# Kernel optimization log

Hardware: AMD Instinct MI355X
Metric: run time of the kernel (lower is better)

Reference implementation:

```python
import math
import jax, jax.numpy as jnp
import numpy as np

B, N, C = 2, 21760, 256
L, Hh, P = 4, 8, 4
Dh = C // Hh


def setup_inputs() -> dict:
    key = jax.random.key(0)
    ks = jax.random.split(key, 8)
    shapes = np.array([[128, 128], [64, 64], [32, 32], [16, 16]], dtype=np.int64)
    areas = shapes[:, 0] * shapes[:, 1]
    start_ids = np.concatenate([[0], np.cumsum(areas)[:-1]]).astype(np.int64)
    S = int(areas.sum())  # 21760

    in_feats = jax.random.normal(ks[0], (B, N, C), jnp.float32)
    sample_priors = jax.random.uniform(ks[1], (B, N, L, 2), jnp.float32)
    sample_feats = jax.random.normal(ks[2], (B, S, C), jnp.float32)

    # sampling_offsets: zero-init weight in torch; use small random so offsets vary,
    # bias is the canonical deformable-DETR grid init.
    W_off = jax.random.normal(ks[3], (C, Hh * L * P * 2), jnp.float32) * 0.01
    thetas = jnp.arange(Hh, dtype=jnp.float32) * (2.0 * math.pi / Hh)
    grid = jnp.stack([jnp.cos(thetas), jnp.sin(thetas)], axis=1)  # [Hh,2]
    grid = grid / jnp.max(jnp.abs(grid), axis=1, keepdims=True)
    grid = jnp.tile(grid[:, None, None, :], (1, L, P, 1))  # [Hh,L,P,2]
    sizes = jnp.arange(1, P + 1, dtype=jnp.float32).reshape(1, 1, P, 1)
    b_off = (sizes * grid).reshape(-1)  # [Hh*L*P*2]

    W_attn = jax.random.normal(ks[4], (C, Hh * L * P), jnp.float32) * 0.01
    b_attn = jnp.zeros((Hh * L * P,), jnp.float32)
    W_val = jax.random.normal(ks[5], (C, C), jnp.float32) / math.sqrt(C)
    b_val = jnp.zeros((C,), jnp.float32)
    W_out = jax.random.normal(ks[6], (C, C), jnp.float32) / math.sqrt(C)
    b_out = jnp.zeros((C,), jnp.float32)

    return dict(in_feats=in_feats, sample_priors=sample_priors, sample_feats=sample_feats,
                sample_map_shapes=jnp.asarray(shapes), sample_map_start_ids=jnp.asarray(start_ids),
                W_off=W_off, b_off=b_off, W_attn=W_attn, b_attn=b_attn,
                W_val=W_val, b_val=b_val, W_out=W_out, b_out=b_out)


def _msda_core(value, shapes_np, starts_np, loc, attn_w):
    """value: [B,S,Hh,Dh]; loc: [B,N,Hh,L,P,2] in [0,1]; attn_w: [B,N,Hh,L,P].
    Bilinear sampling matching grid_sample(align_corners=False, padding='zeros')."""
    b, n = loc.shape[:2]
    acc = jnp.zeros((b, n, Hh, Dh), value.dtype)
    for l in range(L):
        H_l, W_l = int(shapes_np[l, 0]), int(shapes_np[l, 1])
        s0 = int(starts_np[l])
        v = value[:, s0:s0 + H_l * W_l]  # [B,S_l,Hh,Dh]
        lx = loc[:, :, :, l, :, 0] * W_l - 0.5  # [B,N,Hh,P] pixel coords
        ly = loc[:, :, :, l, :, 1] * H_l - 0.5
        x0f, y0f = jnp.floor(lx), jnp.floor(ly)
        wx1, wy1 = lx - x0f, ly - y0f
        wx0, wy0 = 1.0 - wx1, 1.0 - wy1
        x0, y0 = x0f.astype(jnp.int32), y0f.astype(jnp.int32)

        def gather(xi, yi):
            valid = ((xi >= 0) & (xi < W_l) & (yi >= 0) & (yi < H_l)).astype(v.dtype)
            idx = jnp.clip(yi, 0, H_l - 1) * W_l + jnp.clip(xi, 0, W_l - 1)  # [B,N,Hh,P]
            idx_t = idx.transpose(0, 1, 3, 2).reshape(b, n * P, Hh)
            g = jnp.take_along_axis(v, idx_t[..., None], axis=1)  # [B,N*P,Hh,Dh]
            g = g.reshape(b, n, P, Hh, Dh).transpose(0, 1, 3, 2, 4)  # [B,N,Hh,P,Dh]
            return g * valid[..., None]

        samp = (gather(x0, y0) * (wx0 * wy0)[..., None]
                + gather(x0 + 1, y0) * (wx1 * wy0)[..., None]
                + gather(x0, y0 + 1) * (wx0 * wy1)[..., None]
                + gather(x0 + 1, y0 + 1) * (wx1 * wy1)[..., None])
        acc = acc + jnp.einsum('bnhpd,bnhp->bnhd', samp, attn_w[:, :, :, l, :])
    return acc


def reference(in_feats, sample_priors, sample_feats, sample_map_shapes, sample_map_start_ids,
              W_off, b_off, W_attn, b_attn, W_val, b_val, W_out, b_out):
    b, n = in_feats.shape[:2]
    # structural constants (level geometry)
    shapes_np = np.asarray(jax.device_get(sample_map_shapes))
    starts_np = np.asarray(jax.device_get(sample_map_start_ids))

    off = (in_feats @ W_off + b_off).reshape(b, n, Hh, L, P, 2)
    normalizer = jnp.flip(sample_map_shapes, axis=-1).astype(in_feats.dtype)  # [L,2] (W,H)
    loc = sample_priors[:, :, None, :, None, :] + off / normalizer[None, None, None, :, None, :]

    aw = jax.nn.softmax((in_feats @ W_attn + b_attn).reshape(b, n, Hh, L * P), axis=-1)
    aw = aw.reshape(b, n, Hh, L, P)

    value = (sample_feats @ W_val + b_val).reshape(b, -1, Hh, Dh)
    weighted = _msda_core(value, shapes_np, starts_np, loc, aw)  # [B,N,Hh,Dh]
    out = weighted.reshape(b, n, Hh * Dh) @ W_out + b_out
    return out
```

## Files before the change

kernel.cpp:

```cpp
#include <hip/hip_runtime.h>
#include <cstdint>

constexpr int kB = 2;
constexpr int kN = 21760;
constexpr int kC = 256;
constexpr int kH = 8;
constexpr int kS = 21760;
constexpr int kM = kB * kN;

typedef __attribute__((ext_vector_type(8))) short bf16x8;
typedef __attribute__((ext_vector_type(4))) float f32x4;
typedef __attribute__((ext_vector_type(8))) unsigned short us8;

__device__ __forceinline__ float bf2f(unsigned short u) {
  return __uint_as_float(((unsigned int)u) << 16);
}
__device__ __forceinline__ unsigned short f2bf(float f) {
  unsigned int u = __float_as_uint(f);
  u += 0x7fffu + ((u >> 16) & 1u);
  return (unsigned short)(u >> 16);
}
__device__ __forceinline__ float blo(unsigned int v) { return __uint_as_float(v << 16); }
__device__ __forceinline__ float bhi(unsigned int v) { return __uint_as_float(v & 0xffff0000u); }
__device__ __forceinline__ void gld_lds16(const unsigned short* g, unsigned short* l) {
  __builtin_amdgcn_global_load_lds(
      (const __attribute__((address_space(1))) unsigned int*)g,
      (__attribute__((address_space(3))) unsigned int*)l, 16, 0, 0);
}

__global__ __launch_bounds__(256) void convert_act(
    const float* __restrict__ a, const float* __restrict__ b,
    unsigned short* __restrict__ da, unsigned short* __restrict__ db)
{
  const int tid = blockIdx.x * 256 + threadIdx.x;
  const int half = kM * 32;
  const float* src; unsigned short* dst; int id;
  if (tid < half) { src = a; dst = da; id = tid; }
  else            { src = b; dst = db; id = tid - half; }
  const int m = id >> 5;
  const int kb = (id & 31) * 8;
  const float4 x0 = *(const float4*)&src[(size_t)m * 256 + kb];
  const float4 x1 = *(const float4*)&src[(size_t)m * 256 + kb + 4];
  us8 o;
  o[0] = f2bf(x0.x); o[1] = f2bf(x0.y); o[2] = f2bf(x0.z); o[3] = f2bf(x0.w);
  o[4] = f2bf(x1.x); o[5] = f2bf(x1.y); o[6] = f2bf(x1.z); o[7] = f2bf(x1.w);
  *(us8*)&dst[(size_t)m * 256 + (kb ^ ((m & 7) << 3))] = o;
}

__global__ __launch_bounds__(256) void prep_weights(
    const float* __restrict__ Woff, const float* __restrict__ Wattn,
    const float* __restrict__ Wval, const float* __restrict__ Wout,
    unsigned short* __restrict__ BtOff, unsigned short* __restrict__ BtAttn,
    unsigned short* __restrict__ BtVal, unsigned short* __restrict__ BtOut)
{
  const int tid = blockIdx.x * 256 + threadIdx.x;
  const int r = tid >> 5;
  const int kb = (tid & 31) * 8;
  const float* W; unsigned short* Bt; int n, Nn;
  if (r < 256)      { W = Woff;  Bt = BtOff;  n = r;       Nn = 256; }
  else if (r < 384) { W = Wattn; Bt = BtAttn; n = r - 256; Nn = 128; }
  else if (r < 640) { W = Wval;  Bt = BtVal;  n = r - 384; Nn = 256; }
  else              { W = Wout;  Bt = BtOut;  n = r - 640; Nn = 256; }
  us8 o;
#pragma unroll
  for (int i = 0; i < 8; ++i) o[i] = f2bf(W[(size_t)(kb + i) * Nn + n]);
  *(us8*)&Bt[(size_t)n * 256 + (kb ^ ((n & 7) << 3))] = o;
}

template <int OMODE>
__global__ __launch_bounds__(256) void gemm_bf16(
    const unsigned short* __restrict__ A,
    const unsigned short* __restrict__ Bt,
    const float* __restrict__ bias,
    void* __restrict__ Cout, int Nn)
{
  __shared__ unsigned short As[128 * 64];
  __shared__ unsigned short Bs[128 * 64];
  const int t = threadIdx.x;
  const int w = t >> 6, l = t & 63;
  const int m0 = blockIdx.x * 128, n0 = blockIdx.y * 128;
  const int wm = w >> 1, wn = w & 1;

  f32x4 acc[4][4] = {};

  const int srow = l >> 3;
  const int skb  = (l & 7) * 8;

  for (int kt = 0; kt < 256; kt += 64) {
#pragma unroll
    for (int i = 0; i < 4; ++i) {
      const int c = i * 4 + w;
      const int row = c * 8 + srow;
      gld_lds16(A + (size_t)(m0 + row) * 256 + kt + skb, &As[c * 512]);
    }
#pragma unroll
    for (int i = 0; i < 4; ++i) {
      const int c = i * 4 + w;
      const int row = c * 8 + srow;
      gld_lds16(Bt + (size_t)(n0 + row) * 256 + kt + skb, &Bs[c * 512]);
    }
    __syncthreads();

#pragma unroll
    for (int s = 0; s < 2; ++s) {
      bf16x8 af[4], bfr[4];
      const int kf = s * 32 + ((l >> 4) * 8);
#pragma unroll
      for (int i = 0; i < 4; ++i) {
        const int row = wm * 64 + i * 16 + (l & 15);
        af[i] = *(const bf16x8*)&As[row * 64 + (kf ^ ((row & 7) << 3))];
      }
#pragma unroll
      for (int j = 0; j < 4; ++j) {
        const int col = wn * 64 + j * 16 + (l & 15);
        bfr[j] = *(const bf16x8*)&Bs[col * 64 + (kf ^ ((col & 7) << 3))];
      }
#pragma unroll
      for (int i = 0; i < 4; ++i)
#pragma unroll
        for (int j = 0; j < 4; ++j)
          acc[i][j] = __builtin_amdgcn_mfma_f32_16x16x32_bf16(af[i], bfr[j], acc[i][j], 0, 0, 0);
    }
    __syncthreads();
  }

  const int lr = l >> 4;
#pragma unroll
  for (int j = 0; j < 4; ++j) {
    const int col = n0 + wn * 64 + j * 16 + (l & 15);
    const float bv = bias[col];
#pragma unroll
    for (int i = 0; i < 4; ++i) {
      const int rbase = m0 + wm * 64 + i * 16 + lr * 4;
#pragma unroll
      for (int r = 0; r < 4; ++r) {
        const float v = acc[i][j][r] + bv;
        const int row = rbase + r;
        if (OMODE == 0) {
          ((float*)Cout)[(size_t)row * Nn + col] = v;
        } else if (OMODE == 1) {
          ((unsigned short*)Cout)[(size_t)row * Nn + col] = f2bf(v);
        } else if (OMODE == 2) {
          const int bb = row >= kS;
          const int s2 = row - bb * kS;
          ((unsigned short*)Cout)[((size_t)(bb * 8 + (col >> 5)) * kS + s2) * 32 + (col & 31)] = f2bf(v);
        } else if (OMODE == 3) {
          ((unsigned short*)Cout)[((size_t)(col >> 4) * kM + row) * 16 + (col & 15)] = f2bf(v);
        } else {
          ((unsigned short*)Cout)[((size_t)(col >> 5) * kM + row) * 32 + (col & 31)] = f2bf(v);
        }
      }
    }
  }
}

__global__ __launch_bounds__(256) void msda_kernel(
    const unsigned short* __restrict__ off_hm,
    const unsigned short* __restrict__ attn_hm,
    const unsigned short* __restrict__ val_bf,
    const float* __restrict__ priors,
    unsigned short* __restrict__ wgt)
{
  __shared__ int s_rec[16 * 136];
  const int bid = blockIdx.x;
  const int plane = bid & 15;
  const int chunk = bid >> 4;
  const int b = plane >> 3, h = plane & 7;
  const int t = threadIdx.x;
  const int ql = t >> 4;
  const int q = b * kN + chunk * 16 + ql;

  {
    const int j = t & 15;
    const int lv = j >> 2;

    const float lgt = bf2f(attn_hm[((size_t)h * kM + q) * 16 + j]);
    float mx = lgt;
#pragma unroll
    for (int m = 8; m; m >>= 1) mx = fmaxf(mx, __shfl_xor(mx, m, 16));
    const float p = __expf(lgt - mx);
    float sum = p;
#pragma unroll
    for (int m = 8; m; m >>= 1) sum += __shfl_xor(sum, m, 16);
    const float wN = p / sum;

    const unsigned int oo = *(const unsigned int*)&off_hm[((size_t)h * kM + q) * 32 + j * 2];
    const float ox = blo(oo);
    const float oy = bhi(oo);
    const float2 pr = *(const float2*)&priors[(size_t)q * 8 + lv * 2];

    const int Wl = 128 >> lv;
    const float fW = (float)Wl;
    const float lx = fmaf(pr.x, fW, ox) - 0.5f;
    const float ly = fmaf(pr.y, fW, oy) - 0.5f;
    const float x0f = floorf(lx), y0f = floorf(ly);
    const float wx1 = lx - x0f, wy1 = ly - y0f;
    const float wx0 = 1.f - wx1, wy0 = 1.f - wy1;
    const int x0 = (int)x0f, y0 = (int)y0f;
    const int start = (int)((0x5400500040000000ull >> (16 * lv)) & 0xffff);

    const bool vx0 = (x0 >= 0) & (x0 < Wl);
    const bool vx1 = (x0 + 1 >= 0) & (x0 + 1 < Wl);
    const bool vy0 = (y0 >= 0) & (y0 < Wl);
    const bool vy1 = (y0 + 1 >= 0) & (y0 + 1 < Wl);
    const int xc0 = min(max(x0, 0), Wl - 1);
    const int xc1 = min(max(x0 + 1, 0), Wl - 1);
    const int yc0 = min(max(y0, 0), Wl - 1);
    const int yc1 = min(max(y0 + 1, 0), Wl - 1);

    const int rt = start + yc0 * Wl;
    const int rb = start + yc1 * Wl;

    int4 r0, r1;
    r0.x = (rt + xc0) * 64; r0.y = __float_as_int((vx0 & vy0) ? wN * wx0 * wy0 : 0.f);
    r0.z = (rt + xc1) * 64; r0.w = __float_as_int((vx1 & vy0) ? wN * wx1 * wy0 : 0.f);
    r1.x = (rb + xc0) * 64; r1.y = __float_as_int((vx0 & vy1) ? wN * wx0 * wy1 : 0.f);
    r1.z = (rb + xc1) * 64; r1.w = __float_as_int((vx1 & vy1) ? wN * wx1 * wy1 : 0.f);

    const int base = ql * 136 + j * 8;
    *(int4*)&s_rec[base] = r0;
    *(int4*)&s_rec[base + 4] = r1;
  }
  __syncthreads();

  const int lane = t & 15;
  const int c = lane >> 2;
  const int k = lane & 3;
  const char* plane_base = (const char*)val_bf + (size_t)plane * kS * 64 + k * 16;
  const int* rp = &s_rec[ql * 136 + c * 2];

  float a0 = 0.f, a1 = 0.f, a2 = 0.f, a3 = 0.f;
  float a4 = 0.f, a5 = 0.f, a6 = 0.f, a7 = 0.f;
#pragma unroll
  for (int j = 0; j < 16; ++j) {
    const int2 r = *(const int2*)&rp[j * 8];
    const float w = __int_as_float(r.y);
    const uint4 v = *(const uint4*)(plane_base + r.x);
    a0 = fmaf(w, blo(v.x), a0); a1 = fmaf(w, bhi(v.x), a1);
    a2 = fmaf(w, blo(v.y), a2); a3 = fmaf(w, bhi(v.y), a3);
    a4 = fmaf(w, blo(v.z), a4); a5 = fmaf(w, bhi(v.z), a5);
    a6 = fmaf(w, blo(v.w), a6); a7 = fmaf(w, bhi(v.w), a7);
  }

#pragma unroll
  for (int m = 4; m <= 8; m <<= 1) {
    a0 += __shfl_xor(a0, m); a1 += __shfl_xor(a1, m);
    a2 += __shfl_xor(a2, m); a3 += __shfl_xor(a3, m);
    a4 += __shfl_xor(a4, m); a5 += __shfl_xor(a5, m);
    a6 += __shfl_xor(a6, m); a7 += __shfl_xor(a7, m);
  }

  if (c == 0) {
    const int c0 = h * 32 + k * 8;
    const int dst = c0 ^ ((q & 7) << 3);
    uint4 o;
    o.x = (unsigned int)f2bf(a0) | ((unsigned int)f2bf(a1) << 16);
    o.y = (unsigned int)f2bf(a2) | ((unsigned int)f2bf(a3) << 16);
    o.z = (unsigned int)f2bf(a4) | ((unsigned int)f2bf(a5) << 16);
    o.w = (unsigned int)f2bf(a6) | ((unsigned int)f2bf(a7) << 16);
    *(uint4*)&wgt[(size_t)q * 256 + dst] = o;
  }
}

extern "C" void kernel_launch(void* const* d_in, const int* in_sizes, int n_in,
                              void* d_out, int out_size, void* d_ws, size_t ws_size,
                              hipStream_t stream) {
  const float* in_feats = (const float*)d_in[0];
  const float* priors   = (const float*)d_in[1];
  const float* sfeats   = (const float*)d_in[2];
  const float* W_off  = (const float*)d_in[5];
  const float* b_off  = (const float*)d_in[6];
  const float* W_attn = (const float*)d_in[7];
  const float* b_attn = (const float*)d_in[8];
  const float* W_val  = (const float*)d_in[9];
  const float* b_val  = (const float*)d_in[10];
  const float* W_out  = (const float*)d_in[11];
  const float* b_out  = (const float*)d_in[12];
  float* out = (float*)d_out;

  unsigned short* in_bf   = (unsigned short*)d_ws;
  unsigned short* s_bf    = in_bf   + (size_t)kM * 256;
  unsigned short* off_bf  = s_bf    + (size_t)kM * 256;
  unsigned short* attn_bf = off_bf  + (size_t)kM * 256;
  unsigned short* val_bf  = attn_bf + (size_t)kM * 128;
  unsigned short* wgt_bf  = val_bf  + (size_t)kM * 256;
  unsigned short* BtOff   = wgt_bf  + (size_t)kM * 256;
  unsigned short* BtAttn  = BtOff   + 256 * 256;
  unsigned short* BtVal   = BtAttn  + 128 * 256;
  unsigned short* BtOut   = BtVal   + 256 * 256;

  const dim3 blk(256);

  convert_act<<<dim3(kM * 32 * 2 / 256), blk, 0, stream>>>(in_feats, sfeats, in_bf, s_bf);
  prep_weights<<<dim3(896 * 32 / 256), blk, 0, stream>>>(
      W_off, W_attn, W_val, W_out, BtOff, BtAttn, BtVal, BtOut);

  gemm_bf16<4><<<dim3(kM / 128, 2), blk, 0, stream>>>(in_bf, BtOff, b_off, off_bf, 256);
  gemm_bf16<3><<<dim3(kM / 128, 1), blk, 0, stream>>>(in_bf, BtAttn, b_attn, attn_bf, 128);
  gemm_bf16<2><<<dim3(kM / 128, 2), blk, 0, stream>>>(s_bf, BtVal, b_val, val_bf, 256);

  msda_kernel<<<dim3(kM / 2), blk, 0, stream>>>(off_bf, attn_bf, val_bf, priors, wgt_bf);

  gemm_bf16<0><<<dim3(kM / 128, 2), blk, 0, stream>>>(wgt_bf, BtOut, b_out, out, 256);
}
```

Baseline: 152.6 us.

## Fuse fp32-to-bf16 conversion into GEMM loads and merge offset/attention GEMMs

Removes the separate activation conversion kernel: the projection GEMMs now read fp32 inputs directly, convert them to bf16 in registers with a packed convert instruction, and write them into swizzled LDS. The offset and attention projections are merged into one launch with three N tiles that share the A tile. Block indices are remapped so that groups of 8 M tiles share an N column. This cuts launches and the round trip of bf16 activations through memory, at the cost of register-staged A loads that replace the asynchronous global-to-LDS loads and of reading fp32 A more than once per N tile.

```diff
diff --git a/kernel.cpp b/kernel.cpp
--- a/kernel.cpp
+++ b/kernel.cpp
@@ -7,6 +7,7 @@
 constexpr int kH = 8;
 constexpr int kS = 21760;
 constexpr int kM = kB * kN;
+constexpr int kMT = 340;
 
 typedef __attribute__((ext_vector_type(8))) short bf16x8;
 typedef __attribute__((ext_vector_type(4))) float f32x4;
@@ -22,29 +23,15 @@
 }
 __device__ __forceinline__ float blo(unsigned int v) { return __uint_as_float(v << 16); }
 __device__ __forceinline__ float bhi(unsigned int v) { return __uint_as_float(v & 0xffff0000u); }
+__device__ __forceinline__ unsigned int cvt_pk_bf16(float lo, float hi) {
+  unsigned int r;
+  asm("v_cvt_pk_bf16_f32 %0, %1, %2" : "=v"(r) : "v"(lo), "v"(hi));
+  return r;
+}
 __device__ __forceinline__ void gld_lds16(const unsigned short* g, unsigned short* l) {
   __builtin_amdgcn_global_load_lds(
       (const __attribute__((address_space(1))) unsigned int*)g,
       (__attribute__((address_space(3))) unsigned int*)l, 16, 0, 0);
-}
-
-__global__ __launch_bounds__(256) void convert_act(
-    const float* __restrict__ a, const float* __restrict__ b,
-    unsigned short* __restrict__ da, unsigned short* __restrict__ db)
-{
-  const int tid = blockIdx.x * 256 + threadIdx.x;
-  const int half = kM * 32;
-  const float* src; unsigned short* dst; int id;
-  if (tid < half) { src = a; dst = da; id = tid; }
-  else            { src = b; dst = db; id = tid - half; }
-  const int m = id >> 5;
-  const int kb = (id & 31) * 8;
-  const float4 x0 = *(const float4*)&src[(size_t)m * 256 + kb];
-  const float4 x1 = *(const float4*)&src[(size_t)m * 256 + kb + 4];
-  us8 o;
-  o[0] = f2bf(x0.x); o[1] = f2bf(x0.y); o[2] = f2bf(x0.z); o[3] = f2bf(x0.w);
-  o[4] = f2bf(x1.x); o[5] = f2bf(x1.y); o[6] = f2bf(x1.z); o[7] = f2bf(x1.w);
-  *(us8*)&dst[(size_t)m * 256 + (kb ^ ((m & 7) << 3))] = o;
 }
 
 __global__ __launch_bounds__(256) void prep_weights(
@@ -67,18 +54,27 @@
   *(us8*)&Bt[(size_t)n * 256 + (kb ^ ((n & 7) << 3))] = o;
 }
 
-template <int OMODE>
-__global__ __launch_bounds__(256) void gemm_bf16(
-    const unsigned short* __restrict__ A,
+template <int KIND>
+__global__ __launch_bounds__(256) void gemm_top(
+    const void* __restrict__ Aip,
     const unsigned short* __restrict__ Bt,
-    const float* __restrict__ bias,
-    void* __restrict__ Cout, int Nn)
+    const float* __restrict__ bias0, const float* __restrict__ bias1,
+    void* __restrict__ out0, void* __restrict__ out1)
 {
+  constexpr int NT = (KIND == 0) ? 3 : 2;
+  const int bid = blockIdx.x;
+  const int x = bid & 7;
+  const int slot = bid >> 3;
+  const int nt = slot % NT;
+  const int mh = slot / NT;
+  const int m = mh * 8 + x;
+  if (m >= kMT) return;
+  const int m0 = m * 128, n0 = nt * 128;
+
   __shared__ unsigned short As[128 * 64];
   __shared__ unsigned short Bs[128 * 64];
   const int t = threadIdx.x;
   const int w = t >> 6, l = t & 63;
-  const int m0 = blockIdx.x * 128, n0 = blockIdx.y * 128;
   const int wm = w >> 1, wn = w & 1;
 
   f32x4 acc[4][4] = {};
@@ -86,12 +82,33 @@
   const int srow = l >> 3;
   const int skb  = (l & 7) * 8;
 
+  const int arow = t >> 1;
+  const int akh  = (t & 1) << 5;
+  const float* af = (const float*)Aip + (size_t)(m0 + arow) * 256 + akh;
+  const unsigned short* abf = (const unsigned short*)Aip;
+
   for (int kt = 0; kt < 256; kt += 64) {
-#pragma unroll
-    for (int i = 0; i < 4; ++i) {
-      const int c = i * 4 + w;
-      const int row = c * 8 + srow;
-      gld_lds16(A + (size_t)(m0 + row) * 256 + kt + skb, &As[c * 512]);
+    if (KIND == 2) {
+#pragma unroll
+      for (int i = 0; i < 4; ++i) {
+        const int c = i * 4 + w;
+        const int row = c * 8 + srow;
+        gld_lds16(abf + (size_t)(m0 + row) * 256 + kt + skb, &As[c * 512]);
+      }
+    } else {
+      float4 f[8];
+#pragma unroll
+      for (int i = 0; i < 8; ++i) f[i] = *(const float4*)&af[kt + i * 4];
+      unsigned int u[16];
+#pragma unroll
+      for (int i = 0; i < 16; ++i)
+        u[i] = cvt_pk_bf16(f[i >> 1][(i & 1) * 2], f[i >> 1][(i & 1) * 2 + 1]);
+      const int swz = (arow & 7) << 3;
+#pragma unroll
+      for (int i = 0; i < 4; ++i) {
+        uint4 o; o.x = u[i*4]; o.y = u[i*4+1]; o.z = u[i*4+2]; o.w = u[i*4+3];
+        *(uint4*)&As[arow * 64 + ((akh + 8 * i) ^ swz)] = o;
+      }
     }
 #pragma unroll
     for (int i = 0; i < 4; ++i) {
@@ -103,12 +120,12 @@
 
 #pragma unroll
     for (int s = 0; s < 2; ++s) {
-      bf16x8 af[4], bfr[4];
+      bf16x8 afr[4], bfr[4];
       const int kf = s * 32 + ((l >> 4) * 8);
 #pragma unroll
       for (int i = 0; i < 4; ++i) {
         const int row = wm * 64 + i * 16 + (l & 15);
-        af[i] = *(const bf16x8*)&As[row * 64 + (kf ^ ((row & 7) << 3))];
+        afr[i] = *(const bf16x8*)&As[row * 64 + (kf ^ ((row & 7) << 3))];
       }
 #pragma unroll
       for (int j = 0; j < 4; ++j) {
@@ -119,7 +136,7 @@
       for (int i = 0; i < 4; ++i)
 #pragma unroll
         for (int j = 0; j < 4; ++j)
-          acc[i][j] = __builtin_amdgcn_mfma_f32_16x16x32_bf16(af[i], bfr[j], acc[i][j], 0, 0, 0);
+          acc[i][j] = __builtin_amdgcn_mfma_f32_16x16x32_bf16(afr[i], bfr[j], acc[i][j], 0, 0, 0);
     }
     __syncthreads();
   }
@@ -128,7 +145,7 @@
 #pragma unroll
   for (int j = 0; j < 4; ++j) {
     const int col = n0 + wn * 64 + j * 16 + (l & 15);
-    const float bv = bias[col];
+    const float bv = (KIND == 0 && n0 == 256) ? bias1[col - 256] : bias0[col];
 #pragma unroll
     for (int i = 0; i < 4; ++i) {
       const int rbase = m0 + wm * 64 + i * 16 + lr * 4;
@@ -136,18 +153,17 @@
       for (int r = 0; r < 4; ++r) {
         const float v = acc[i][j][r] + bv;
         const int row = rbase + r;
-        if (OMODE == 0) {
-          ((float*)Cout)[(size_t)row * Nn + col] = v;
-        } else if (OMODE == 1) {
-          ((unsigned short*)Cout)[(size_t)row * Nn + col] = f2bf(v);
-        } else if (OMODE == 2) {
+        if (KIND == 2) {
+          ((float*)out0)[(size_t)row * 256 + col] = v;
+        } else if (KIND == 1) {
           const int bb = row >= kS;
           const int s2 = row - bb * kS;
-          ((unsigned short*)Cout)[((size_t)(bb * 8 + (col >> 5)) * kS + s2) * 32 + (col & 31)] = f2bf(v);
-        } else if (OMODE == 3) {
-          ((unsigned short*)Cout)[((size_t)(col >> 4) * kM + row) * 16 + (col & 15)] = f2bf(v);
+          ((unsigned short*)out0)[((size_t)(bb * 8 + (col >> 5)) * kS + s2) * 32 + (col & 31)] = f2bf(v);
+        } else if (col < 256) {
+          ((unsigned short*)out0)[((size_t)(col >> 5) * kM + row) * 32 + (col & 31)] = f2bf(v);
         } else {
-          ((unsigned short*)Cout)[((size_t)(col >> 5) * kM + row) * 32 + (col & 31)] = f2bf(v);
+          const int c2 = col - 256;
+          ((unsigned short*)out1)[((size_t)(c2 >> 4) * kM + row) * 16 + (c2 & 15)] = f2bf(v);
         }
       }
     }
@@ -278,11 +294,9 @@
   const float* b_out  = (const float*)d_in[12];
   float* out = (float*)d_out;
 
-  unsigned short* in_bf   = (unsigned short*)d_ws;
-  unsigned short* s_bf    = in_bf   + (size_t)kM * 256;
-  unsigned short* off_bf  = s_bf    + (size_t)kM * 256;
-  unsigned short* attn_bf = off_bf  + (size_t)kM * 256;
-  unsigned short* val_bf  = attn_bf + (size_t)kM * 128;
+  unsigned short* off_hm  = (unsigned short*)d_ws;
+  unsigned short* attn_hm = off_hm  + (size_t)kM * 256;
+  unsigned short* val_bf  = attn_hm + (size_t)kM * 128;
   unsigned short* wgt_bf  = val_bf  + (size_t)kM * 256;
   unsigned short* BtOff   = wgt_bf  + (size_t)kM * 256;
   unsigned short* BtAttn  = BtOff   + 256 * 256;
@@ -291,15 +305,16 @@
 
   const dim3 blk(256);
 
-  convert_act<<<dim3(kM * 32 * 2 / 256), blk, 0, stream>>>(in_feats, sfeats, in_bf, s_bf);
-  prep_weights<<<dim3(896 * 32 / 256), blk, 0, stream>>>(
+  prep_weights<<<dim3(112), blk, 0, stream>>>(
       W_off, W_attn, W_val, W_out, BtOff, BtAttn, BtVal, BtOut);
 
-  gemm_bf16<4><<<dim3(kM / 128, 2), blk, 0, stream>>>(in_bf, BtOff, b_off, off_bf, 256);
-  gemm_bf16<3><<<dim3(kM / 128, 1), blk, 0, stream>>>(in_bf, BtAttn, b_attn, attn_bf, 128);
-  gemm_bf16<2><<<dim3(kM / 128, 2), blk, 0, stream>>>(s_bf, BtVal, b_val, val_bf, 256);
-
-  msda_kernel<<<dim3(kM / 2), blk, 0, stream>>>(off_bf, attn_bf, val_bf, priors, wgt_bf);
-
-  gemm_bf16<0><<<dim3(kM / 128, 2), blk, 0, stream>>>(wgt_bf, BtOut, b_out, out, 256);
-}
+  gemm_top<0><<<dim3(8 * 3 * 43), blk, 0, stream>>>(
+      in_feats, BtOff, b_off, b_attn, off_hm, attn_hm);
+  gemm_top<1><<<dim3(8 * 2 * 43), blk, 0, stream>>>(
+      sfeats, BtVal, b_val, nullptr, val_bf, nullptr);
+
+  msda_kernel<<<dim3(kM / 2), blk, 0, stream>>>(off_hm, attn_hm, val_bf, priors, wgt_bf);
+
+  gemm_top<2><<<dim3(8 * 2 * 43), blk, 0, stream>>>(
+      wgt_bf, BtOut, b_out, nullptr, out, nullptr);
+}
```

New measurement: 159.5 us. +4.5%, slower.

## Merge conversion kernels and fuse leading GEMMs into one launch with XCD-aware tiling

Applied to the files above, without the earlier changes.

Merges activation conversion and weight preparation into a single kernel. The offset, attention and value projections now run as one GEMM launch, which treats BtOff and BtAttn as one contiguous 384-wide weight and picks the bias and output layout per column. Block indices are remapped so that consecutive blocks (bid&7) land on different M tiles, which looks like XCD-aware placement aimed at L2 reuse. The intent is fewer launches and better fill of the GPU, at the cost of more branching in the epilogue.

```diff
diff --git a/kernel.cpp b/kernel.cpp
--- a/kernel.cpp
+++ b/kernel.cpp
@@ -7,6 +7,7 @@
 constexpr int kH = 8;
 constexpr int kS = 21760;
 constexpr int kM = kB * kN;
+constexpr int kMT = 340;
 
 typedef __attribute__((ext_vector_type(8))) short bf16x8;
 typedef __attribute__((ext_vector_type(4))) float f32x4;
@@ -28,61 +29,52 @@
       (__attribute__((address_space(3))) unsigned int*)l, 16, 0, 0);
 }
 
-__global__ __launch_bounds__(256) void convert_act(
+__global__ __launch_bounds__(256) void convprep(
     const float* __restrict__ a, const float* __restrict__ b,
-    unsigned short* __restrict__ da, unsigned short* __restrict__ db)
-{
-  const int tid = blockIdx.x * 256 + threadIdx.x;
-  const int half = kM * 32;
-  const float* src; unsigned short* dst; int id;
-  if (tid < half) { src = a; dst = da; id = tid; }
-  else            { src = b; dst = db; id = tid - half; }
-  const int m = id >> 5;
-  const int kb = (id & 31) * 8;
-  const float4 x0 = *(const float4*)&src[(size_t)m * 256 + kb];
-  const float4 x1 = *(const float4*)&src[(size_t)m * 256 + kb + 4];
-  us8 o;
-  o[0] = f2bf(x0.x); o[1] = f2bf(x0.y); o[2] = f2bf(x0.z); o[3] = f2bf(x0.w);
-  o[4] = f2bf(x1.x); o[5] = f2bf(x1.y); o[6] = f2bf(x1.z); o[7] = f2bf(x1.w);
-  *(us8*)&dst[(size_t)m * 256 + (kb ^ ((m & 7) << 3))] = o;
-}
-
-__global__ __launch_bounds__(256) void prep_weights(
+    unsigned short* __restrict__ da, unsigned short* __restrict__ db,
     const float* __restrict__ Woff, const float* __restrict__ Wattn,
     const float* __restrict__ Wval, const float* __restrict__ Wout,
     unsigned short* __restrict__ BtOff, unsigned short* __restrict__ BtAttn,
     unsigned short* __restrict__ BtVal, unsigned short* __restrict__ BtOut)
 {
-  const int tid = blockIdx.x * 256 + threadIdx.x;
-  const int r = tid >> 5;
-  const int kb = (tid & 31) * 8;
-  const float* W; unsigned short* Bt; int n, Nn;
-  if (r < 256)      { W = Woff;  Bt = BtOff;  n = r;       Nn = 256; }
-  else if (r < 384) { W = Wattn; Bt = BtAttn; n = r - 256; Nn = 128; }
-  else if (r < 640) { W = Wval;  Bt = BtVal;  n = r - 384; Nn = 256; }
-  else              { W = Wout;  Bt = BtOut;  n = r - 640; Nn = 256; }
-  us8 o;
-#pragma unroll
-  for (int i = 0; i < 8; ++i) o[i] = f2bf(W[(size_t)(kb + i) * Nn + n]);
-  *(us8*)&Bt[(size_t)n * 256 + (kb ^ ((n & 7) << 3))] = o;
-}
-
-template <int OMODE>
-__global__ __launch_bounds__(256) void gemm_bf16(
-    const unsigned short* __restrict__ A,
-    const unsigned short* __restrict__ Bt,
-    const float* __restrict__ bias,
-    void* __restrict__ Cout, int Nn)
-{
-  __shared__ unsigned short As[128 * 64];
-  __shared__ unsigned short Bs[128 * 64];
-  const int t = threadIdx.x;
+  const int bid = blockIdx.x;
+  if (bid < 10880) {
+    const int tid = bid * 256 + threadIdx.x;
+    const int half = kM * 32;
+    const float* src; unsigned short* dst; int id;
+    if (tid < half) { src = a; dst = da; id = tid; }
+    else            { src = b; dst = db; id = tid - half; }
+    const int m = id >> 5;
+    const int kb = (id & 31) * 8;
+    const float4 x0 = *(const float4*)&src[(size_t)m * 256 + kb];
+    const float4 x1 = *(const float4*)&src[(size_t)m * 256 + kb + 4];
+    us8 o;
+    o[0] = f2bf(x0.x); o[1] = f2bf(x0.y); o[2] = f2bf(x0.z); o[3] = f2bf(x0.w);
+    o[4] = f2bf(x1.x); o[5] = f2bf(x1.y); o[6] = f2bf(x1.z); o[7] = f2bf(x1.w);
+    *(us8*)&dst[(size_t)m * 256 + (kb ^ ((m & 7) << 3))] = o;
+  } else {
+    const int tid = (bid - 10880) * 256 + threadIdx.x;
+    const int r = tid >> 5;
+    const int kb = (tid & 31) * 8;
+    const float* W; unsigned short* Bt; int n, Nn;
+    if (r < 256)      { W = Woff;  Bt = BtOff;  n = r;       Nn = 256; }
+    else if (r < 384) { W = Wattn; Bt = BtAttn; n = r - 256; Nn = 128; }
+    else if (r < 640) { W = Wval;  Bt = BtVal;  n = r - 384; Nn = 256; }
+    else              { W = Wout;  Bt = BtOut;  n = r - 640; Nn = 256; }
+    us8 o;
+#pragma unroll
+    for (int i = 0; i < 8; ++i) o[i] = f2bf(W[(size_t)(kb + i) * Nn + n]);
+    *(us8*)&Bt[(size_t)n * 256 + (kb ^ ((n & 7) << 3))] = o;
+  }
+}
+
+__device__ __forceinline__ void mfma_tile_256(
+    const unsigned short* __restrict__ A, const unsigned short* __restrict__ Bt,
+    int m0, int n0, int t, unsigned short* As, unsigned short* Bs,
+    f32x4 (&acc)[4][4])
+{
   const int w = t >> 6, l = t & 63;
-  const int m0 = blockIdx.x * 128, n0 = blockIdx.y * 128;
   const int wm = w >> 1, wn = w & 1;
-
-  f32x4 acc[4][4] = {};
-
   const int srow = l >> 3;
   const int skb  = (l & 7) * 8;
 
@@ -103,12 +95,12 @@
 
 #pragma unroll
     for (int s = 0; s < 2; ++s) {
-      bf16x8 af[4], bfr[4];
+      bf16x8 afr[4], bfr[4];
       const int kf = s * 32 + ((l >> 4) * 8);
 #pragma unroll
       for (int i = 0; i < 4; ++i) {
         const int row = wm * 64 + i * 16 + (l & 15);
-        af[i] = *(const bf16x8*)&As[row * 64 + (kf ^ ((row & 7) << 3))];
+        afr[i] = *(const bf16x8*)&As[row * 64 + (kf ^ ((row & 7) << 3))];
       }
 #pragma unroll
       for (int j = 0; j < 4; ++j) {
@@ -119,16 +111,47 @@
       for (int i = 0; i < 4; ++i)
 #pragma unroll
         for (int j = 0; j < 4; ++j)
-          acc[i][j] = __builtin_amdgcn_mfma_f32_16x16x32_bf16(af[i], bfr[j], acc[i][j], 0, 0, 0);
+          acc[i][j] = __builtin_amdgcn_mfma_f32_16x16x32_bf16(afr[i], bfr[j], acc[i][j], 0, 0, 0);
     }
     __syncthreads();
   }
-
+}
+
+__global__ __launch_bounds__(256) void gemm_lead(
+    const unsigned short* __restrict__ in_bf,
+    const unsigned short* __restrict__ s_bf,
+    const unsigned short* __restrict__ BtOA,
+    const unsigned short* __restrict__ BtVal,
+    const float* __restrict__ b_off, const float* __restrict__ b_attn,
+    const float* __restrict__ b_val,
+    unsigned short* __restrict__ off_hm,
+    unsigned short* __restrict__ attn_hm,
+    unsigned short* __restrict__ val_hm)
+{
+  const int bid = blockIdx.x;
+  const int x = bid & 7;
+  const int slot = bid >> 3;
+  int mode, nt, mh;
+  if (slot < 129) { mode = 0; nt = slot % 3; mh = slot / 3; }
+  else            { mode = 1; const int s2 = slot - 129; nt = s2 % 2; mh = s2 / 2; }
+  const int m = mh * 8 + x;
+  if (m >= kMT) return;
+  const int m0 = m * 128, n0 = nt * 128;
+
+  __shared__ unsigned short As[128 * 64];
+  __shared__ unsigned short Bs[128 * 64];
+  const int t = threadIdx.x;
+
+  f32x4 acc[4][4] = {};
+  mfma_tile_256(mode ? s_bf : in_bf, mode ? BtVal : BtOA, m0, n0, t, As, Bs, acc);
+
+  const int w = t >> 6, l = t & 63;
+  const int wm = w >> 1, wn = w & 1;
   const int lr = l >> 4;
 #pragma unroll
   for (int j = 0; j < 4; ++j) {
     const int col = n0 + wn * 64 + j * 16 + (l & 15);
-    const float bv = bias[col];
+    const float bv = mode ? b_val[col] : (col < 256 ? b_off[col] : b_attn[col - 256]);
 #pragma unroll
     for (int i = 0; i < 4; ++i) {
       const int rbase = m0 + wm * 64 + i * 16 + lr * 4;
@@ -136,20 +159,56 @@
       for (int r = 0; r < 4; ++r) {
         const float v = acc[i][j][r] + bv;
         const int row = rbase + r;
-        if (OMODE == 0) {
-          ((float*)Cout)[(size_t)row * Nn + col] = v;
-        } else if (OMODE == 1) {
-          ((unsigned short*)Cout)[(size_t)row * Nn + col] = f2bf(v);
-        } else if (OMODE == 2) {
+        if (mode == 1) {
           const int bb = row >= kS;
           const int s2 = row - bb * kS;
-          ((unsigned short*)Cout)[((size_t)(bb * 8 + (col >> 5)) * kS + s2) * 32 + (col & 31)] = f2bf(v);
-        } else if (OMODE == 3) {
-          ((unsigned short*)Cout)[((size_t)(col >> 4) * kM + row) * 16 + (col & 15)] = f2bf(v);
+          val_hm[((size_t)(bb * 8 + (col >> 5)) * kS + s2) * 32 + (col & 31)] = f2bf(v);
+        } else if (col < 256) {
+          off_hm[((size_t)(col >> 5) * kM + row) * 32 + (col & 31)] = f2bf(v);
         } else {
-          ((unsigned short*)Cout)[((size_t)(col >> 5) * kM + row) * 32 + (col & 31)] = f2bf(v);
+          const int c2 = col - 256;
+          attn_hm[((size_t)(c2 >> 4) * kM + row) * 16 + (c2 & 15)] = f2bf(v);
         }
       }
+    }
+  }
+}
+
+__global__ __launch_bounds__(256) void gemm_out(
+    const unsigned short* __restrict__ wgt,
+    const unsigned short* __restrict__ BtOut,
+    const float* __restrict__ b_out,
+    float* __restrict__ out)
+{
+  const int bid = blockIdx.x;
+  const int x = bid & 7;
+  const int slot = bid >> 3;
+  const int nt = slot % 2;
+  const int mh = slot / 2;
+  const int m = mh * 8 + x;
+  if (m >= kMT) return;
+  const int m0 = m * 128, n0 = nt * 128;
+
+  __shared__ unsigned short As[128 * 64];
+  __shared__ unsigned short Bs[128 * 64];
+  const int t = threadIdx.x;
+
+  f32x4 acc[4][4] = {};
+  mfma_tile_256(wgt, BtOut, m0, n0, t, As, Bs, acc);
+
+  const int w = t >> 6, l = t & 63;
+  const int wm = w >> 1, wn = w & 1;
+  const int lr = l >> 4;
+#pragma unroll
+  for (int j = 0; j < 4; ++j) {
+    const int col = n0 + wn * 64 + j * 16 + (l & 15);
+    const float bv = b_out[col];
+#pragma unroll
+    for (int i = 0; i < 4; ++i) {
+      const int rbase = m0 + wm * 64 + i * 16 + lr * 4;
+#pragma unroll
+      for (int r = 0; r < 4; ++r)
+        out[(size_t)(rbase + r) * 256 + col] = acc[i][j][r] + bv;
     }
   }
 }
@@ -280,10 +339,10 @@
 
   unsigned short* in_bf   = (unsigned short*)d_ws;
   unsigned short* s_bf    = in_bf   + (size_t)kM * 256;
-  unsigned short* off_bf  = s_bf    + (size_t)kM * 256;
-  unsigned short* attn_bf = off_bf  + (size_t)kM * 256;
-  unsigned short* val_bf  = attn_bf + (size_t)kM * 128;
-  unsigned short* wgt_bf  = val_bf  + (size_t)kM * 256;
+  unsigned short* off_hm  = s_bf    + (size_t)kM * 256;
+  unsigned short* attn_hm = off_hm  + (size_t)kM * 256;
+  unsigned short* val_hm  = attn_hm + (size_t)kM * 128;
+  unsigned short* wgt_bf  = val_hm  + (size_t)kM * 256;
   unsigned short* BtOff   = wgt_bf  + (size_t)kM * 256;
   unsigned short* BtAttn  = BtOff   + 256 * 256;
   unsigned short* BtVal   = BtAttn  + 128 * 256;
@@ -291,15 +350,14 @@
 
   const dim3 blk(256);
 
-  convert_act<<<dim3(kM * 32 * 2 / 256), blk, 0, stream>>>(in_feats, sfeats, in_bf, s_bf);
-  prep_weights<<<dim3(896 * 32 / 256), blk, 0, stream>>>(
+  convprep<<<dim3(10992), blk, 0, stream>>>(
+      in_feats, sfeats, in_bf, s_bf,
       W_off, W_attn, W_val, W_out, BtOff, BtAttn, BtVal, BtOut);
 
-  gemm_bf16<4><<<dim3(kM / 128, 2), blk, 0, stream>>>(in_bf, BtOff, b_off, off_bf, 256);
-  gemm_bf16<3><<<dim3(kM / 128, 1), blk, 0, stream>>>(in_bf, BtAttn, b_attn, attn_bf, 128);
-  gemm_bf16<2><<<dim3(kM / 128, 2), blk, 0, stream>>>(s_bf, BtVal, b_val, val_bf, 256);
-
-  msda_kernel<<<dim3(kM / 2), blk, 0, stream>>>(off_bf, attn_bf, val_bf, priors, wgt_bf);
-
-  gemm_bf16<0><<<dim3(kM / 128, 2), blk, 0, stream>>>(wgt_bf, BtOut, b_out, out, 256);
-}
+  gemm_lead<<<dim3(8 * 215), blk, 0, stream>>>(
+      in_bf, s_bf, BtOff, BtVal, b_off, b_attn, b_val, off_hm, attn_hm, val_hm);
+
+  msda_kernel<<<dim3(kM / 2), blk, 0, stream>>>(off_hm, attn_hm, val_hm, priors, wgt_bf);
+
+  gemm_out<<<dim3(8 * 2 * 43), blk, 0, stream>>>(wgt_bf, BtOut, b_out, out);
+}
```

Measured after the change: 150.9 us. No clear change (-1.1%).
